# Optimization experiments

Hardware: AMD Instinct MI355X
Metric: run time of the kernel (lower is better)

Reference implementation:

```python
import jax, jax.numpy as jnp
import numpy as np

NUM_BEAM, NUM_NULL, NUM_BIN, NUM_CH = 8, 4, 257, 8
NUM_BLOCK, NUM_FRAME = 8, 500
ALPHA, LOW_FREQ, HIGH_FREQ = 0.35, 5, 70


def setup_inputs() -> dict:
    key = jax.random.key(0)
    k1, k2, k3, k4 = jax.random.split(key, 4)
    return {
        "input": jax.random.normal(k1, (NUM_BLOCK, NUM_FRAME, 2, NUM_BIN, NUM_CH), jnp.float32),
        "beam_id": jax.random.randint(k2, (NUM_BLOCK,), 0, NUM_BEAM),
        "targ_w": jax.random.normal(k3, (NUM_BEAM, 2, NUM_BIN, NUM_CH), jnp.float32),
        "null_w": jax.random.normal(k4, (NUM_BEAM, NUM_NULL, 2, NUM_BIN, NUM_CH), jnp.float32),
    }


def _forward(input, beam_id, targ_w, null_w):
    a = ALPHA
    xr, xi = input[:, :, 0], input[:, :, 1]            # (B,T,F,C)
    # target beamformer: select per-block complex weights (B,2,F,C)
    tw = targ_w[beam_id]
    twr, twi = tw[:, 0], tw[:, 1]                      # (B,F,C)
    tr = jnp.einsum('btfc,bfc->btf', xr, twr) - jnp.einsum('btfc,bfc->btf', xi, twi)
    ti = jnp.einsum('btfc,bfc->btf', xr, twi) + jnp.einsum('btfc,bfc->btf', xi, twr)
    tr, ti = tr[..., None], ti[..., None]              # (B,T,F,1)
    # null beamformer: (B,N,2,F,C)
    nw = null_w[beam_id]
    nwr, nwi = nw[:, :, 0], nw[:, :, 1]                # (B,N,F,C)
    nr = jnp.einsum('btfc,bnfc->btfn', xr, nwr) - jnp.einsum('btfc,bnfc->btfn', xi, nwi)
    ni = jnp.einsum('btfc,bnfc->btfn', xr, nwi) + jnp.einsum('btfc,bnfc->btfn', xi, nwr)
    # elementwise cross-spectra products (B,T,F,N)
    pr = tr * nr + ti * ni
    pi = ti * nr - tr * ni
    pw = jnp.mean(xr ** 2 + xi ** 2, axis=-1, keepdims=True)  # (B,T,F,1)

    # t = 0 (note: (1-alpha) scales only the FIRST product, as in the source)
    phi_r0 = (1.0 - a) * tr[:, 0] * nr[:, 0] + ti[:, 0] * ni[:, 0]
    phi_i0 = (1.0 - a) * ti[:, 0] * nr[:, 0] - tr[:, 0] * ni[:, 0]
    psd0 = (1.0 - a) * pw[:, 0]
    phi0 = jnp.sqrt(phi_r0 ** 2 + phi_i0 ** 2)
    dcf0 = jnp.clip(phi0 / (psd0 + 1e-13), 0.01, 1.0)

    def step(carry, xs):
        phi_r, phi_i, psd = carry
        pr_t, pi_t, pw_t = xs
        phi_r = a * phi_r + (1.0 - a) * pr_t
        phi_i = a * phi_i + (1.0 - a) * pi_t
        psd = a * psd + (1.0 - a) * pw_t
        phi = jnp.sqrt(phi_r ** 2 + phi_i ** 2)
        dcf_t = jnp.clip(phi / (psd + 1e-13), 0.01, 1.0)
        pre = jnp.sum(psd[:, LOW_FREQ:HIGH_FREQ, :], axis=1, keepdims=True)
        aft = jnp.sum(phi[:, LOW_FREQ:HIGH_FREQ, :], axis=1, keepdims=True)
        ratio = jnp.clip(aft / (pre + 1e-10), 0.01, 1.0)
        dcf_t = jnp.sqrt(dcf_t * ratio)
        return (phi_r, phi_i, psd), dcf_t

    xs = (jnp.moveaxis(pr[:, 1:], 1, 0),
          jnp.moveaxis(pi[:, 1:], 1, 0),
          jnp.moveaxis(pw[:, 1:], 1, 0))
    _, dcf_rest = jax.lax.scan(step, (phi_r0, phi_i0, psd0), xs)  # (T-1,B,F,N)
    dcf = jnp.concatenate([dcf0[None], dcf_rest], axis=0)
    dcf = jnp.moveaxis(dcf, 0, 1)                                 # (B,T,F,N)
    targ_out = jnp.stack([tr[..., 0], ti[..., 0]], axis=2)        # (B,T,2,F)
    return dcf, targ_out


def reference(input, beam_id, targ_w, null_w):
    return _forward(input, beam_id, targ_w, null_w)
```

## Files before the change

kernel.cpp:

```cpp
#include <hip/hip_runtime.h>

#define NB 8
#define NT 500
#define NF 257
#define NC 8
#define NNUL 4
#define LOWF 5
#define HIGHF 70
#define S_CHUNK 8
#define WARM 8
#define N_CHUNK 63
#define AL 0.35f

__device__ __forceinline__ float dot8(const float4& a0, const float4& a1,
                                      const float4& b0, const float4& b1) {
    return a0.x*b0.x + a0.y*b0.y + a0.z*b0.z + a0.w*b0.w
         + a1.x*b1.x + a1.y*b1.y + a1.z*b1.z + a1.w*b1.w;
}

__global__ __launch_bounds__(512, 2) void dcf_ema_kernel(
    const float* __restrict__ x,
    const int* __restrict__ beam_id,
    const float* __restrict__ targ_w,
    const float* __restrict__ null_w,
    float* __restrict__ out,
    float* __restrict__ ws)
{
    const int tid = threadIdx.x;
    const int bid = blockIdx.x;
    const int fh = bid & 1;
    const int b  = (bid >> 1) & 7;
    const int k  = bid >> 4;
    const int t0 = k * S_CHUNK;
    const int te = min(NT, t0 + S_CHUNK);
    int ts = t0 - WARM; if (ts < 0) ts = 0;

    const int f = fh * 128 + (tid >> 2);
    const int n = tid & 3;
    const int wid = tid >> 6;
    const int lane = tid & 63;
    const bool extra = (fh == 1) && (tid < 4);

    __shared__ float s_w256[16 + 4 * 16];

    const int beam = beam_id[b];
    const int pA = n & 1;
    const int offA = pA * (NF * NC);
    const int offB = (1 - pA) * (NF * NC);
    const int psel = (n == 1 || n == 2) ? 1 : 0;
    const float nsign = pA ? -1.f : 1.f;

    float4 tw0, tw1, nwA0, nwA1, nwB0, nwB1;
    {
        const float* tp = targ_w + ((size_t)(beam * 2 + psel) * NF + f) * NC;
        tw0 = *(const float4*)(tp);  tw1 = *(const float4*)(tp + 4);
        const float* qp = null_w + ((size_t)((beam * NNUL + n) * 2) * NF + f) * NC;
        nwA0 = *(const float4*)(qp + offA);  nwA1 = *(const float4*)(qp + offA + 4);
        nwB0 = *(const float4*)(qp + offB);  nwB1 = *(const float4*)(qp + offB + 4);
    }
    if (tid < 16) {
        int p = tid >> 3, c = tid & 7;
        s_w256[tid] = targ_w[((size_t)(beam * 2 + p) * NF + 256) * NC + c];
    } else if (tid < 80) {
        int i = tid - 16;
        int nn = i >> 4, p = (i >> 3) & 1, c = i & 7;
        s_w256[tid] = null_w[((size_t)((beam * NNUL + nn) * 2 + p) * NF + 256) * NC + c];
    }
    __syncthreads();

    float phi_r = 0.f, phi_i = 0.f, psd = 0.f;
    float phi_r2 = 0.f, phi_i2 = 0.f, psd2 = 0.f;
    const float a = AL, oma = 1.0f - AL;
    const size_t rowlen = 2 * NF * NC;
    const bool in_red = (f >= LOWF) && (f < HIGHF);

    const float* xrow = x + (size_t)(b * NT + ts) * rowlen + f * NC;
    float4 pA0 = *(const float4*)(xrow + offA);
    float4 pA1 = *(const float4*)(xrow + offA + 4);
    float4 pB0 = *(const float4*)(xrow + offB);
    float4 pB1 = *(const float4*)(xrow + offB + 4);

    float* outT = out + (size_t)NB * NT * NF * NNUL;

    for (int t = ts; t < te; ++t) {
        const float4 A0 = pA0, A1 = pA1, B0 = pB0, B1 = pB1;
        if (t + 1 < te) {
            const float* xr2 = x + (size_t)(b * NT + t + 1) * rowlen + f * NC;
            pA0 = *(const float4*)(xr2 + offA);
            pA1 = *(const float4*)(xr2 + offA + 4);
            pB0 = *(const float4*)(xr2 + offB);
            pB1 = *(const float4*)(xr2 + offB + 4);
        }

        const float d = dot8(A0, A1, tw0, tw1);
        const float e = __shfl_xor(d, 1);
        const float u = (n < 2) ? ((n == 0) ? (d - e) : (e - d)) : (d + e);
        const float v = __shfl_xor(u, 2);
        const float tr = (n < 2) ? u : v;
        const float ti = (n < 2) ? v : u;

        const float P = dot8(A0, A1, nwA0, nwA1);
        const float Q = dot8(B0, B1, nwB0, nwB1);
        const float nr = nsign * (P - Q);
        const float ni = dot8(A0, A1, nwB0, nwB1) + dot8(B0, B1, nwA0, nwA1);
        const float pw = (dot8(A0, A1, A0, A1) + dot8(B0, B1, B0, B1)) * 0.125f;

        if (t == 0) {
            phi_r = oma * tr * nr + ti * ni;
            phi_i = oma * ti * nr - tr * ni;
            psd   = oma * pw;
        } else {
            phi_r = a * phi_r + oma * (tr * nr + ti * ni);
            phi_i = a * phi_i + oma * (ti * nr - tr * ni);
            psd   = a * psd + oma * pw;
        }

        float tr2 = 0.f, ti2 = 0.f;
        if (extra) {
            const float* xw = x + (size_t)(b * NT + t) * rowlen + 256 * NC;
            const float4 eA0 = *(const float4*)(xw + offA);
            const float4 eA1 = *(const float4*)(xw + offA + 4);
            const float4 eB0 = *(const float4*)(xw + offB);
            const float4 eB1 = *(const float4*)(xw + offB + 4);
            const float4 etw0 = *(const float4*)&s_w256[psel * 8];
            const float4 etw1 = *(const float4*)&s_w256[psel * 8 + 4];
            const float* nq = &s_w256[16 + n * 16];
            const float4 enA0 = *(const float4*)(nq + pA * 8);
            const float4 enA1 = *(const float4*)(nq + pA * 8 + 4);
            const float4 enB0 = *(const float4*)(nq + (1 - pA) * 8);
            const float4 enB1 = *(const float4*)(nq + (1 - pA) * 8 + 4);
            const float d2 = dot8(eA0, eA1, etw0, etw1);
            const float e2 = __shfl_xor(d2, 1);
            const float u2 = (n < 2) ? ((n == 0) ? (d2 - e2) : (e2 - d2)) : (d2 + e2);
            const float v2 = __shfl_xor(u2, 2);
            tr2 = (n < 2) ? u2 : v2;
            ti2 = (n < 2) ? v2 : u2;
            const float P2 = dot8(eA0, eA1, enA0, enA1);
            const float Q2 = dot8(eB0, eB1, enB0, enB1);
            const float nr2 = nsign * (P2 - Q2);
            const float ni2 = dot8(eA0, eA1, enB0, enB1) + dot8(eB0, eB1, enA0, enA1);
            const float pw2 = (dot8(eA0, eA1, eA0, eA1) + dot8(eB0, eB1, eB0, eB1)) * 0.125f;
            if (t == 0) {
                phi_r2 = oma * tr2 * nr2 + ti2 * ni2;
                phi_i2 = oma * ti2 * nr2 - tr2 * ni2;
                psd2   = oma * pw2;
            } else {
                phi_r2 = a * phi_r2 + oma * (tr2 * nr2 + ti2 * ni2);
                phi_i2 = a * phi_i2 + oma * (ti2 * nr2 - tr2 * ni2);
                psd2   = a * psd2 + oma * pw2;
            }
        }

        if (t >= t0) {
            const float phi = sqrtf(phi_r * phi_r + phi_i * phi_i);
            const float dcfv = fminf(fmaxf(phi / (psd + 1e-13f), 0.01f), 1.0f);
            const size_t bt = (size_t)(b * NT + t);
            out[(bt * NF + f) * NNUL + n] = dcfv;
            if (n == 0) outT[(bt * 2 + 0) * NF + f] = tr;
            if (n == 1) outT[(bt * 2 + 1) * NF + f] = ti;
            if (extra) {
                const float phi2 = sqrtf(phi_r2 * phi_r2 + phi_i2 * phi_i2);
                const float dcf2v = fminf(fmaxf(phi2 / (psd2 + 1e-13f), 0.01f), 1.0f);
                out[(bt * NF + 256) * NNUL + n] = dcf2v;
                if (n == 0) outT[(bt * 2 + 0) * NF + 256] = tr2;
                if (n == 1) outT[(bt * 2 + 1) * NF + 256] = ti2;
            }
            if (fh == 0 && t >= 1 && wid < 5) {
                float v_phi = in_red ? phi : 0.f;
                float v_psd = (in_red && n == 0) ? psd : 0.f;
                #pragma unroll
                for (int off = 4; off < 64; off <<= 1) {
                    v_phi += __shfl_xor(v_phi, off);
                    v_psd += __shfl_xor(v_psd, off);
                }
                float* cell = ws + bt * 5;
                if (lane < 4) atomicAdd(cell + lane, v_phi);
                if (lane == 0) atomicAdd(cell + 4, v_psd);
            }
        }
    }
}

__global__ __launch_bounds__(256) void dcf_ratio_kernel(
    float* __restrict__ out, const float* __restrict__ ws)
{
    const int bt = blockIdx.x;
    if ((bt % NT) == 0) return;
    __shared__ float s_ratio[4];
    if (threadIdx.x < 4) {
        const float pre = ws[bt * 5 + 4];
        const float aft = ws[bt * 5 + threadIdx.x];
        s_ratio[threadIdx.x] = fminf(fmaxf(aft / (pre + 1e-10f), 0.01f), 1.0f);
    }
    __syncthreads();
    const float r0 = s_ratio[0], r1 = s_ratio[1], r2 = s_ratio[2], r3 = s_ratio[3];
    float4* dcf = (float4*)(out + (size_t)bt * (NF * NNUL));
    for (int i = threadIdx.x; i < NF; i += 256) {
        float4 v = dcf[i];
        v.x = sqrtf(v.x * r0);
        v.y = sqrtf(v.y * r1);
        v.z = sqrtf(v.z * r2);
        v.w = sqrtf(v.w * r3);
        dcf[i] = v;
    }
}

extern "C" void kernel_launch(void* const* d_in, const int* in_sizes, int n_in,
                              void* d_out, int out_size, void* d_ws, size_t ws_size,
                              hipStream_t stream) {
    const float* x       = (const float*)d_in[0];
    const int*   beam_id = (const int*)d_in[1];
    const float* targ_w  = (const float*)d_in[2];
    const float* null_w  = (const float*)d_in[3];
    float* out           = (float*)d_out;
    float* ws            = (float*)d_ws;

    hipMemsetAsync(ws, 0, (size_t)NB * NT * 5 * sizeof(float), stream);
    dcf_ema_kernel<<<dim3(NB * N_CHUNK * 2), dim3(512), 0, stream>>>(
        x, beam_id, targ_w, null_w, out, ws);
    dcf_ratio_kernel<<<dim3(NB * NT), dim3(256), 0, stream>>>(out, ws);
}
```

Measured before the change: 147.3 us.

## Deepen input prefetch to three frames and rebalance time chunks with shorter warmup

Replaces the one-frame register prefetch of input rows with a three-deep rotating register pipeline, so more global loads are in flight per thread. Time chunks grow from 8 to 10 frames with warmup cut from 8 to 6, which reduces redundant warmup recomputation and the block count. The risks are higher register pressure under the 512-thread, 2-block launch bound, and a warmup of 6 EMA steps (0.35^6) that may loosen accuracy. The bound clamp on te is removed on the assumption that 50 chunks of 10 divide 500 exactly, and the initial loads read three rows unconditionally.

```diff
diff --git a/kernel.cpp b/kernel.cpp
--- a/kernel.cpp
+++ b/kernel.cpp
@@ -7,9 +7,9 @@
 #define NNUL 4
 #define LOWF 5
 #define HIGHF 70
-#define S_CHUNK 8
-#define WARM 8
-#define N_CHUNK 63
+#define S_CHUNK 10
+#define WARM 6
+#define N_CHUNK 50
 #define AL 0.35f
 
 __device__ __forceinline__ float dot8(const float4& a0, const float4& a1,
@@ -32,7 +32,7 @@
     const int b  = (bid >> 1) & 7;
     const int k  = bid >> 4;
     const int t0 = k * S_CHUNK;
-    const int te = min(NT, t0 + S_CHUNK);
+    const int te = t0 + S_CHUNK;
     int ts = t0 - WARM; if (ts < 0) ts = 0;
 
     const int f = fh * 128 + (tid >> 2);
@@ -74,36 +74,49 @@
     const size_t rowlen = 2 * NF * NC;
     const bool in_red = (f >= LOWF) && (f < HIGHF);
 
-    const float* xrow = x + (size_t)(b * NT + ts) * rowlen + f * NC;
-    float4 pA0 = *(const float4*)(xrow + offA);
-    float4 pA1 = *(const float4*)(xrow + offA + 4);
-    float4 pB0 = *(const float4*)(xrow + offB);
-    float4 pB1 = *(const float4*)(xrow + offB + 4);
+    const float* xp = x + (size_t)(b * NT + ts) * rowlen + f * NC;
+    float4 aA0 = *(const float4*)(xp + offA);
+    float4 aA1 = *(const float4*)(xp + offA + 4);
+    float4 aB0 = *(const float4*)(xp + offB);
+    float4 aB1 = *(const float4*)(xp + offB + 4);
+    xp += rowlen;
+    float4 bA0 = *(const float4*)(xp + offA);
+    float4 bA1 = *(const float4*)(xp + offA + 4);
+    float4 bB0 = *(const float4*)(xp + offB);
+    float4 bB1 = *(const float4*)(xp + offB + 4);
+    xp += rowlen;
+    float4 cA0 = *(const float4*)(xp + offA);
+    float4 cA1 = *(const float4*)(xp + offA + 4);
+    float4 cB0 = *(const float4*)(xp + offB);
+    float4 cB1 = *(const float4*)(xp + offB + 4);
+    xp += rowlen;
 
     float* outT = out + (size_t)NB * NT * NF * NNUL;
 
+    #pragma unroll 3
     for (int t = ts; t < te; ++t) {
-        const float4 A0 = pA0, A1 = pA1, B0 = pB0, B1 = pB1;
-        if (t + 1 < te) {
-            const float* xr2 = x + (size_t)(b * NT + t + 1) * rowlen + f * NC;
-            pA0 = *(const float4*)(xr2 + offA);
-            pA1 = *(const float4*)(xr2 + offA + 4);
-            pB0 = *(const float4*)(xr2 + offB);
-            pB1 = *(const float4*)(xr2 + offB + 4);
-        }
-
-        const float d = dot8(A0, A1, tw0, tw1);
+        const float d = dot8(aA0, aA1, tw0, tw1);
         const float e = __shfl_xor(d, 1);
         const float u = (n < 2) ? ((n == 0) ? (d - e) : (e - d)) : (d + e);
         const float v = __shfl_xor(u, 2);
         const float tr = (n < 2) ? u : v;
         const float ti = (n < 2) ? v : u;
 
-        const float P = dot8(A0, A1, nwA0, nwA1);
-        const float Q = dot8(B0, B1, nwB0, nwB1);
+        const float P = dot8(aA0, aA1, nwA0, nwA1);
+        const float Q = dot8(aB0, aB1, nwB0, nwB1);
         const float nr = nsign * (P - Q);
-        const float ni = dot8(A0, A1, nwB0, nwB1) + dot8(B0, B1, nwA0, nwA1);
-        const float pw = (dot8(A0, A1, A0, A1) + dot8(B0, B1, B0, B1)) * 0.125f;
+        const float ni = dot8(aA0, aA1, nwB0, nwB1) + dot8(aB0, aB1, nwA0, nwA1);
+        const float pw = (dot8(aA0, aA1, aA0, aA1) + dot8(aB0, aB1, aB0, aB1)) * 0.125f;
+
+        aA0 = bA0; aA1 = bA1; aB0 = bB0; aB1 = bB1;
+        bA0 = cA0; bA1 = cA1; bB0 = cB0; bB1 = cB1;
+        if (t + 3 < te) {
+            cA0 = *(const float4*)(xp + offA);
+            cA1 = *(const float4*)(xp + offA + 4);
+            cB0 = *(const float4*)(xp + offB);
+            cB1 = *(const float4*)(xp + offB + 4);
+        }
+        xp += rowlen;
 
         if (t == 0) {
             phi_r = oma * tr * nr + ti * ni;
```

Measured after the change: 164.1 us. 1.11x slower.
